# Kernel tuning notes

Measured on AMD Instinct MI355X. Metric: run time of the kernel, lower is better.

The kernel has to match this reference:

```python
import jax, jax.numpy as jnp
import numpy as np

B, S, D, V, T, NS, NG = 16, 512, 400, 32000, 8, 30, 3


def setup_inputs() -> dict:
    key = jax.random.key(0)
    ks = jax.random.split(key, 14)
    w = 1.0 / np.sqrt(D)
    return {
        "encoded_hidden": jax.random.normal(ks[0], (1, B, D), jnp.float32) * 0.1,
        "encoded_outputs": jax.random.normal(ks[1], (B, S, D), jnp.float32) * 0.1,
        "story": jax.random.randint(ks[2], (B, S), 0, V),
        "trg_batches": jax.random.randint(ks[3], (B, NS, T), 0, V),
        "shared_emb": jax.random.normal(ks[4], (V, D), jnp.float32) * 0.1,
        "slot_emb": jax.random.normal(ks[5], (1, D), jnp.float32) * 0.1,
        "w_ih": jax.random.normal(ks[6], (3 * D, D), jnp.float32) * w,
        "w_hh": jax.random.normal(ks[7], (3 * D, D), jnp.float32) * w,
        "b_ih": jax.random.normal(ks[8], (3 * D,), jnp.float32) * w,
        "b_hh": jax.random.normal(ks[9], (3 * D,), jnp.float32) * w,
        "w_ratio_w": jax.random.normal(ks[10], (1, 3 * D), jnp.float32) * w,
        "w_ratio_b": jax.random.normal(ks[11], (1,), jnp.float32) * w,
        "w_gate_w": jax.random.normal(ks[12], (NG, D), jnp.float32) * w,
        "w_gate_b": jax.random.normal(ks[13], (NG,), jnp.float32) * w,
        "batch_size": B,
        "max_resp_len": T,
    }


def reference(encoded_hidden, encoded_outputs, story, trg_batches, shared_emb,
              slot_emb, w_ih, w_hh, b_ih, b_hh, w_ratio_w, w_ratio_b,
              w_gate_w, w_gate_b, batch_size, max_resp_len):
    # Original torch code returns inside the slot loop -> only slot 0 is decoded.
    # h0 is re-used as GRU initial state at EVERY step (no carried hidden), and
    # teacher forcing makes each step's input known, so all T steps vectorize.
    h0 = encoded_hidden[0]                         # (B, D)
    Bq, Tq = batch_size, max_resp_len
    Vq = shared_emb.shape[0]

    # decoder inputs: step 0 = slot embedding, steps 1..T-1 = emb(trg[:,0,i-1])
    x0 = jnp.broadcast_to(slot_emb, h0.shape)      # (B, D)
    xt = shared_emb[trg_batches[:, 0, : Tq - 1]]   # (B, T-1, D)
    X = jnp.concatenate([x0[:, None, :], xt], axis=1)  # (B, T, D)

    # GRU cell (torch gate order r, z, n), h0 broadcast over steps
    gi = X @ w_ih.T + b_ih                         # (B, T, 3D)
    gh = h0 @ w_hh.T + b_hh                        # (B, 3D)
    i_r, i_z, i_n = jnp.split(gi, 3, axis=-1)
    h_r, h_z, h_n = jnp.split(gh, 3, axis=-1)
    r = jax.nn.sigmoid(i_r + h_r[:, None, :])
    z = jax.nn.sigmoid(i_z + h_z[:, None, :])
    n = jnp.tanh(i_n + r * h_n[:, None, :])
    h = (1.0 - z) * n + z * h0[:, None, :]         # (B, T, D) decoder_state == hidden

    # attention over history (no length masking: all lens == S)
    scores = jnp.einsum('btd,bsd->bts', h, encoded_outputs)   # (B, T, S)
    probs = jax.nn.softmax(scores, axis=-1)
    # FAITHFUL to original bug: context uses raw scores, not probs
    context = jnp.einsum('bts,bsd->btd', scores, encoded_outputs)

    gate0 = context[:, 0, :] @ w_gate_w.T + w_gate_b          # (B, NG), step i==0

    p_vocab = jax.nn.softmax(h @ shared_emb.T, axis=-1)       # (B, T, V)
    p_gen = jax.nn.sigmoid(
        jnp.concatenate([h, context, X], axis=-1) @ w_ratio_w.T + w_ratio_b
    )                                                         # (B, T, 1)

    # pointer distribution: scatter_add probs onto vocab ids of the story
    p_ctx = jnp.zeros((Bq, Tq, Vq), p_vocab.dtype).at[
        jnp.arange(Bq)[:, None, None],
        jnp.arange(Tq)[None, :, None],
        story[:, None, :],
    ].add(probs)

    p_final = p_gen * p_vocab + (1.0 - p_gen) * p_ctx         # (B, T, V)

    ptr_outputs = jnp.zeros((NS, Bq, Tq, Vq), p_final.dtype).at[0].set(p_final)
    gate_outputs = jnp.zeros((NS, Bq, NG), gate0.dtype).at[0].set(gate0)
    return ptr_outputs, gate_outputs
```

## Files before the change

### kernel.cpp

```cpp
#include <hip/hip_runtime.h>

#define Bq 16
#define Sq 512
#define Dq 400
#define Vq 32000
#define Tq 8
#define NSq 30
#define NGq 3
#define BTq (Bq*Tq)
#define SLICE 4096000
#define PTR_TOTAL (30ull*SLICE)
#define GATE_TOTAL (NSq*Bq*NGq)

#define ZTOT 29696000ull
#define ZPER 16384
#define AZB 640
#define LZB 1173

#define NCOMPUTE 250

#define FBLK 8
#define FCH (Vq/FBLK)

typedef float f4nt __attribute__((ext_vector_type(4)));

__device__ inline float sigmoidf_(float x) { return 1.0f / (1.0f + __expf(-x)); }

__device__ inline unsigned bf16rne(float x) {
    unsigned u = __float_as_uint(x);
    return (u + 0x7FFFu + ((u >> 16) & 1u)) >> 16;
}

__device__ inline float blockReduceSum(float v, float* red) {
    int tid = threadIdx.x;
    #pragma unroll
    for (int o = 32; o > 0; o >>= 1) v += __shfl_down(v, o, 64);
    if ((tid & 63) == 0) red[tid >> 6] = v;
    __syncthreads();
    if (tid == 0) {
        float s = red[0];
        int nw = blockDim.x >> 6;
        for (int i = 1; i < nw; i++) s += red[i];
        red[0] = s;
    }
    __syncthreads();
    float r = red[0];
    __syncthreads();
    return r;
}

__device__ inline float blockReduceMax(float v, float* red) {
    int tid = threadIdx.x;
    #pragma unroll
    for (int o = 32; o > 0; o >>= 1) v = fmaxf(v, __shfl_down(v, o, 64));
    if ((tid & 63) == 0) red[tid >> 6] = v;
    __syncthreads();
    if (tid == 0) {
        float s = red[0];
        int nw = blockDim.x >> 6;
        for (int i = 1; i < nw; i++) s = fmaxf(s, red[i]);
        red[0] = s;
    }
    __syncthreads();
    float r = red[0];
    __syncthreads();
    return r;
}

__global__ __launch_bounds__(512) void k_attn(const float* __restrict__ enc_hidden,
                                              const float* __restrict__ shared_emb,
                                              const float* __restrict__ slot_emb,
                                              const float* __restrict__ w_ih,
                                              const float* __restrict__ w_hh,
                                              const float* __restrict__ b_ih,
                                              const float* __restrict__ b_hh,
                                              const int* __restrict__ trg,
                                              const float* __restrict__ enc_out,
                                              const int* __restrict__ story,
                                              const float* __restrict__ w_ratio_w,
                                              const float* __restrict__ w_ratio_b,
                                              const float* __restrict__ w_gate_w,
                                              const float* __restrict__ w_gate_b,
                                              float* __restrict__ probs, float* __restrict__ pgen,
                                              float* __restrict__ hT, float* __restrict__ out_gate,
                                              float* __restrict__ out) {
    int tid = threadIdx.x;
    if (blockIdx.x >= BTq) {
        int zb = blockIdx.x - BTq;
        f4nt z = (f4nt)(0.0f);
        f4nt* dst = (f4nt*)(out + (size_t)SLICE);
        size_t base = (size_t)zb * ZPER + tid;
        #pragma unroll
        for (int r = 0; r < ZPER / 512; ++r) {
            size_t idx = base + (size_t)r * 512;
            if (idx < ZTOT) __builtin_nontemporal_store(z, &dst[idx]);
        }
        return;
    }
    __shared__ float x_l[Dq], h0_l[Dq], h_l[Dq], ctx_l[Dq], sc_l[Sq];
    __shared__ float gi_l[1200], gh_l[1200];
    __shared__ float red[8];
    int bt = blockIdx.x, b = bt >> 3, t = bt & 7;
    if (tid < 100) {
        const float4* src = (t == 0) ? (const float4*)slot_emb
            : (const float4*)(shared_emb + (size_t)trg[b * (NSq * Tq) + (t - 1)] * Dq);
        *(float4*)&x_l[4 * tid] = src[tid];
    } else if (tid >= 256 && tid < 356) {
        int q = tid - 256;
        *(float4*)&h0_l[4 * q] = ((const float4*)(enc_hidden + b * Dq))[q];
    }
    __syncthreads();
    for (int j = tid; j < 1200; j += 512) {
        const float4* wi4 = (const float4*)(w_ih + (size_t)j * Dq);
        const float4* wh4 = (const float4*)(w_hh + (size_t)j * Dq);
        const float4* x4  = (const float4*)x_l;
        const float4* h4  = (const float4*)h0_l;
        float ai = b_ih[j], ah = b_hh[j];
        #pragma unroll 4
        for (int q = 0; q < Dq / 4; ++q) {
            float4 wv = wi4[q], av = x4[q];
            ai += av.x * wv.x + av.y * wv.y + av.z * wv.z + av.w * wv.w;
            float4 wh = wh4[q], hv = h4[q];
            ah += hv.x * wh.x + hv.y * wh.y + hv.z * wh.z + hv.w * wh.w;
        }
        gi_l[j] = ai; gh_l[j] = ah;
    }
    __syncthreads();
    if (tid < Dq) {
        int d = tid;
        float r_ = sigmoidf_(gi_l[d] + gh_l[d]);
        float z  = sigmoidf_(gi_l[Dq + d] + gh_l[Dq + d]);
        float n  = tanhf(gi_l[2 * Dq + d] + r_ * gh_l[2 * Dq + d]);
        float h  = (1.0f - z) * n + z * h0_l[d];
        h_l[d] = h;
        hT[d * BTq + bt] = h;
    }
    __syncthreads();
    {
        const float4* e4 = (const float4*)(enc_out + ((size_t)(b * Sq + tid)) * Dq);
        float acc = 0.0f;
        for (int q = 0; q < Dq / 4; ++q) {
            float4 p = e4[q];
            int k = 4 * q;
            acc += h_l[k]*p.x + h_l[k+1]*p.y + h_l[k+2]*p.z + h_l[k+3]*p.w;
        }
        sc_l[tid] = acc;
    }
    __syncthreads();
    float myv = sc_l[tid];
    float m = blockReduceMax(myv, red);
    float e = __expf(myv - m);
    float ssum = blockReduceSum(e, red);
    probs[bt * Sq + tid] = e / ssum;
    for (int d = tid; d < Dq; d += 512) {
        float acc = 0.0f;
        #pragma unroll 8
        for (int s = 0; s < Sq; ++s)
            acc += sc_l[s] * enc_out[((size_t)(b * Sq + s)) * Dq + d];
        ctx_l[d] = acc;
    }
    __syncthreads();
    {
        float part = 0.0f;
        for (int i = tid; i < 1200; i += 512) {
            float v = (i < Dq) ? h_l[i] : (i < 2 * Dq ? ctx_l[i - Dq] : x_l[i - 2 * Dq]);
            part += v * w_ratio_w[i];
        }
        float tot = blockReduceSum(part, red);
        if (tid == 0) pgen[bt] = sigmoidf_(tot + w_ratio_b[0]);
    }
    if (t == 0) {
        for (int g = 0; g < NGq; ++g) {
            float part = 0.0f;
            for (int d = tid; d < Dq; d += 512) part += ctx_l[d] * w_gate_w[g * Dq + d];
            float tot = blockReduceSum(part, red);
            if (tid == 0) out_gate[b * NGq + g] = tot + w_gate_b[g];
        }
    }
}

#define TVL 128
#define CKL 40
__global__ __launch_bounds__(256) void k_logits(const float* __restrict__ hT,
                                                const float* __restrict__ emb,
                                                unsigned short* __restrict__ logits,
                                                float* __restrict__ pmax,
                                                float* __restrict__ psum,
                                                float* __restrict__ out) {
    __shared__ float eT[CKL][132];
    __shared__ float hL[CKL][132];
    int bid = blockIdx.x;
    int tid = threadIdx.x;
    if (bid >= NCOMPUTE) {
        int zl = bid - NCOMPUTE;
        if (zl < LZB) {
            int zb = AZB + zl;
            f4nt z = (f4nt)(0.0f);
            f4nt* dst = (f4nt*)(out + (size_t)SLICE);
            size_t base = (size_t)zb * ZPER + tid;
            #pragma unroll
            for (int r = 0; r < ZPER / 256; ++r) {
                size_t idx = base + (size_t)r * 256;
                if (idx < ZTOT) __builtin_nontemporal_store(z, &dst[idx]);
            }
        } else {
            float4 z4 = make_float4(0.0f, 0.0f, 0.0f, 0.0f);
            float4* g = (float4*)(out + PTR_TOTAL + Bq * NGq);
            for (int i = tid; i < (GATE_TOTAL - Bq * NGq) / 4; i += 256) g[i] = z4;
        }
        return;
    }
    int v0 = bid * TVL;
    int tx = tid & 15, ty = tid >> 4;
    float acc[8][8];
    #pragma unroll
    for (int j = 0; j < 8; ++j)
        #pragma unroll
        for (int i = 0; i < 8; ++i) acc[j][i] = 0.0f;

    for (int c = 0; c < Dq / CKL; ++c) {
        int k0 = c * CKL;
        const float4* hg = (const float4*)(hT + (size_t)k0 * BTq);
        #pragma unroll
        for (int r = 0; r < 5; ++r) {
            int idx = tid + 256 * r;
            int k = idx >> 5, c4 = idx & 31;
            float4 vd = hg[idx];
            *(float4*)&hL[k][4 * c4] = vd;
        }
        #pragma unroll
        for (int r = 0; r < 5; ++r) {
            int idx = tid + 256 * r;
            int v = idx / 10, q = idx - 10 * v;
            float4 vd = *(const float4*)(emb + (size_t)(v0 + v) * Dq + k0 + 4 * q);
            eT[4*q+0][v] = vd.x; eT[4*q+1][v] = vd.y; eT[4*q+2][v] = vd.z; eT[4*q+3][v] = vd.w;
        }
        __syncthreads();
        #pragma unroll 4
        for (int k = 0; k < CKL; ++k) {
            float4 h0 = *(const float4*)&hL[k][8 * ty];
            float4 h1 = *(const float4*)&hL[k][8 * ty + 4];
            float4 e0 = *(const float4*)&eT[k][8 * tx];
            float4 e1 = *(const float4*)&eT[k][8 * tx + 4];
            float hv[8] = {h0.x, h0.y, h0.z, h0.w, h1.x, h1.y, h1.z, h1.w};
            float ev[8] = {e0.x, e0.y, e0.z, e0.w, e1.x, e1.y, e1.z, e1.w};
            #pragma unroll
            for (int j = 0; j < 8; ++j)
                #pragma unroll
                for (int i = 0; i < 8; ++i)
                    acc[j][i] += hv[j] * ev[i];
        }
        __syncthreads();
    }
    #pragma unroll
    for (int j = 0; j < 8; ++j) {
        int bt = 8 * ty + j;
        unsigned bb[8];
        float r[8];
        float m = -1e30f;
        #pragma unroll
        for (int i = 0; i < 8; ++i) {
            bb[i] = bf16rne(acc[j][i]);
            r[i] = __uint_as_float(bb[i] << 16);
            m = fmaxf(m, r[i]);
        }
        #pragma unroll
        for (int o = 8; o >= 1; o >>= 1) m = fmaxf(m, __shfl_xor(m, o, 16));
        float es = 0.0f;
        #pragma unroll
        for (int i = 0; i < 8; ++i) es += __expf(r[i] - m);
        #pragma unroll
        for (int o = 8; o >= 1; o >>= 1) es += __shfl_xor(es, o, 16);
        if (tx == 0) {
            pmax[bid * BTq + bt] = m;
            psum[bid * BTq + bt] = es;
        }
        uint4 w = make_uint4(bb[0] | (bb[1] << 16), bb[2] | (bb[3] << 16),
                             bb[4] | (bb[5] << 16), bb[6] | (bb[7] << 16));
        *(uint4*)(logits + (size_t)bt * Vq + v0 + 8 * tx) = w;
    }
}

__global__ __launch_bounds__(256) void k_final(const unsigned short* __restrict__ logits,
                                               const float* __restrict__ probs,
                                               const int* __restrict__ story,
                                               const float* __restrict__ pgen,
                                               const float* __restrict__ pmax,
                                               const float* __restrict__ psum,
                                               float* __restrict__ out) {
    __shared__ float chunk[FCH];
    __shared__ float red[4];
    int bid = blockIdx.x, tid = threadIdx.x;
    int bt = bid >> 3, ch = bid & 7, b = bt >> 3;
    float pm = (tid < NCOMPUTE) ? pmax[tid * BTq + bt] : -1e30f;
    float m = blockReduceMax(pm, red);
    float part = (tid < NCOMPUTE) ? psum[tid * BTq + bt] * __expf(pm - m) : 0.0f;
    float s = blockReduceSum(part, red);
    float inv = 1.0f / s, pg = pgen[bt], cg = 1.0f - pg;
    int lo = ch * FCH;
    const uint4* l4 = (const uint4*)(logits + (size_t)bt * Vq + lo);
    for (int i = tid; i < FCH / 8; i += 256) {
        uint4 lv = l4[i];
        float f0 = __uint_as_float(lv.x << 16), f1 = __uint_as_float(lv.x & 0xFFFF0000u);
        float f2 = __uint_as_float(lv.y << 16), f3 = __uint_as_float(lv.y & 0xFFFF0000u);
        float f4 = __uint_as_float(lv.z << 16), f5 = __uint_as_float(lv.z & 0xFFFF0000u);
        float f6 = __uint_as_float(lv.w << 16), f7 = __uint_as_float(lv.w & 0xFFFF0000u);
        chunk[8 * i + 0] = pg * __expf(f0 - m) * inv;
        chunk[8 * i + 1] = pg * __expf(f1 - m) * inv;
        chunk[8 * i + 2] = pg * __expf(f2 - m) * inv;
        chunk[8 * i + 3] = pg * __expf(f3 - m) * inv;
        chunk[8 * i + 4] = pg * __expf(f4 - m) * inv;
        chunk[8 * i + 5] = pg * __expf(f5 - m) * inv;
        chunk[8 * i + 6] = pg * __expf(f6 - m) * inv;
        chunk[8 * i + 7] = pg * __expf(f7 - m) * inv;
    }
    __syncthreads();
    for (int ss = tid; ss < Sq; ss += 256) {
        int rel = story[b * Sq + ss] - lo;
        if (rel >= 0 && rel < FCH)
            atomicAdd(&chunk[rel], cg * probs[bt * Sq + ss]);
    }
    __syncthreads();
    f4nt* o4 = (f4nt*)(out + (size_t)bt * Vq + lo);
    const f4nt* c4 = (const f4nt*)chunk;
    for (int i = tid; i < FCH / 4; i += 256)
        __builtin_nontemporal_store(c4[i], &o4[i]);
}

extern "C" void kernel_launch(void* const* d_in, const int* in_sizes, int n_in,
                              void* d_out, int out_size, void* d_ws, size_t ws_size,
                              hipStream_t stream) {
    const float* enc_hidden = (const float*)d_in[0];
    const float* enc_out    = (const float*)d_in[1];
    const int*   story      = (const int*)d_in[2];
    const int*   trg        = (const int*)d_in[3];
    const float* shared_emb = (const float*)d_in[4];
    const float* slot_emb   = (const float*)d_in[5];
    const float* w_ih       = (const float*)d_in[6];
    const float* w_hh       = (const float*)d_in[7];
    const float* b_ih       = (const float*)d_in[8];
    const float* b_hh       = (const float*)d_in[9];
    const float* w_ratio_w  = (const float*)d_in[10];
    const float* w_ratio_b  = (const float*)d_in[11];
    const float* w_gate_w   = (const float*)d_in[12];
    const float* w_gate_b   = (const float*)d_in[13];

    float* out = (float*)d_out;

    float* ws = (float*)d_ws;
    unsigned short* logits_buf = (unsigned short*)ws;
    float* probs_buf  = ws + (size_t)SLICE;
    float* hT_buf     = ws + 2 * (size_t)SLICE;
    float* pgen_buf   = hT_buf + 51200;
    float* pmax_buf   = pgen_buf + 128;
    float* psum_buf   = pmax_buf + 32000;

    hipLaunchKernelGGL(k_attn, dim3(BTq + AZB), dim3(512), 0, stream,
                       enc_hidden, shared_emb, slot_emb, w_ih, w_hh, b_ih, b_hh, trg,
                       enc_out, story, w_ratio_w, w_ratio_b, w_gate_w, w_gate_b,
                       probs_buf, pgen_buf, hT_buf, out + PTR_TOTAL, out);
    hipLaunchKernelGGL(k_logits, dim3(NCOMPUTE + LZB + 1), dim3(256), 0, stream,
                       hT_buf, shared_emb, logits_buf, pmax_buf, psum_buf, out);
    hipLaunchKernelGGL(k_final, dim3(BTq * FBLK), dim3(256), 0, stream,
                       logits_buf, probs_buf, story, pgen_buf, pmax_buf, psum_buf, out);
}
```

Baseline: 735.7 us.

## Fuse logits and final softmax/scatter via cooperative grid sync, drop bf16 logits buffer

Merges the logits GEMM and the final softmax-plus-pointer-scatter kernel into one cooperative kernel. Logits stay in registers across a grid-wide sync, so the bf16 logits buffer no longer has to be written and re-read. Each block reduces the global max/sum, then applies the softmax, does the story scatter into its 128-wide vocab slice and writes the output. The zero-fill blocks become a fixed grid-stride set that also joins the grid sync. The costs are a cooperative launch with a limit on grid size, a grid barrier, and a per-block scatter loop over all 128 rows × 512 story tokens.

```diff
diff --git a/kernel.cpp b/kernel.cpp
--- a/kernel.cpp
+++ b/kernel.cpp
@@ -1,4 +1,5 @@
 #include <hip/hip_runtime.h>
+#include <hip/hip_cooperative_groups.h>
 
 #define Bq 16
 #define Sq 512
@@ -15,12 +16,11 @@
 #define ZTOT 29696000ull
 #define ZPER 16384
 #define AZB 640
-#define LZB 1173
+#define ZSTART (640ull*16384ull)
 
 #define NCOMPUTE 250
-
-#define FBLK 8
-#define FCH (Vq/FBLK)
+#define NZB 262
+#define ZSTRIDE (NZB*256)
 
 typedef float f4nt __attribute__((ext_vector_type(4)));
 
@@ -181,38 +181,39 @@
 
 #define TVL 128
 #define CKL 40
-__global__ __launch_bounds__(256) void k_logits(const float* __restrict__ hT,
-                                                const float* __restrict__ emb,
-                                                unsigned short* __restrict__ logits,
-                                                float* __restrict__ pmax,
-                                                float* __restrict__ psum,
-                                                float* __restrict__ out) {
-    __shared__ float eT[CKL][132];
-    __shared__ float hL[CKL][132];
+__global__ __launch_bounds__(256, 2) void k_logits(const float* __restrict__ hT,
+                                                   const float* __restrict__ emb,
+                                                   const float* __restrict__ probs,
+                                                   const int* __restrict__ story,
+                                                   const float* __restrict__ pgen,
+                                                   float* __restrict__ pmax,
+                                                   float* __restrict__ psum,
+                                                   float* __restrict__ out) {
+    namespace cg = cooperative_groups;
+    __shared__ __align__(16) float smem[16384];
     int bid = blockIdx.x;
     int tid = threadIdx.x;
+    int tx = tid & 15, ty = tid >> 4;
+    int v0 = bid * TVL;
+    float acc[8][8];
+
     if (bid >= NCOMPUTE) {
-        int zl = bid - NCOMPUTE;
-        if (zl < LZB) {
-            int zb = AZB + zl;
-            f4nt z = (f4nt)(0.0f);
-            f4nt* dst = (f4nt*)(out + (size_t)SLICE);
-            size_t base = (size_t)zb * ZPER + tid;
-            #pragma unroll
-            for (int r = 0; r < ZPER / 256; ++r) {
-                size_t idx = base + (size_t)r * 256;
-                if (idx < ZTOT) __builtin_nontemporal_store(z, &dst[idx]);
-            }
-        } else {
+        int zb = bid - NCOMPUTE;
+        f4nt z = (f4nt)(0.0f);
+        f4nt* dst = (f4nt*)(out + (size_t)SLICE);
+        for (size_t idx = ZSTART + (size_t)zb * 256 + tid; idx < ZTOT; idx += ZSTRIDE)
+            __builtin_nontemporal_store(z, &dst[idx]);
+        if (zb == 0) {
             float4 z4 = make_float4(0.0f, 0.0f, 0.0f, 0.0f);
             float4* g = (float4*)(out + PTR_TOTAL + Bq * NGq);
             for (int i = tid; i < (GATE_TOTAL - Bq * NGq) / 4; i += 256) g[i] = z4;
         }
+        cg::this_grid().sync();
         return;
     }
-    int v0 = bid * TVL;
-    int tx = tid & 15, ty = tid >> 4;
-    float acc[8][8];
+
+    float (*eT)[132] = (float(*)[132])smem;
+    float (*hL)[132] = (float(*)[132])(smem + 5280);
     #pragma unroll
     for (int j = 0; j < 8; ++j)
         #pragma unroll
@@ -255,76 +256,84 @@
     #pragma unroll
     for (int j = 0; j < 8; ++j) {
         int bt = 8 * ty + j;
-        unsigned bb[8];
-        float r[8];
         float m = -1e30f;
         #pragma unroll
         for (int i = 0; i < 8; ++i) {
-            bb[i] = bf16rne(acc[j][i]);
-            r[i] = __uint_as_float(bb[i] << 16);
-            m = fmaxf(m, r[i]);
+            unsigned bb = bf16rne(acc[j][i]);
+            acc[j][i] = __uint_as_float(bb << 16);
+            m = fmaxf(m, acc[j][i]);
         }
         #pragma unroll
         for (int o = 8; o >= 1; o >>= 1) m = fmaxf(m, __shfl_xor(m, o, 16));
         float es = 0.0f;
         #pragma unroll
-        for (int i = 0; i < 8; ++i) es += __expf(r[i] - m);
+        for (int i = 0; i < 8; ++i) es += __expf(acc[j][i] - m);
         #pragma unroll
         for (int o = 8; o >= 1; o >>= 1) es += __shfl_xor(es, o, 16);
         if (tx == 0) {
-            pmax[bid * BTq + bt] = m;
-            psum[bid * BTq + bt] = es;
-        }
-        uint4 w = make_uint4(bb[0] | (bb[1] << 16), bb[2] | (bb[3] << 16),
-                             bb[4] | (bb[5] << 16), bb[6] | (bb[7] << 16));
-        *(uint4*)(logits + (size_t)bt * Vq + v0 + 8 * tx) = w;
-    }
-}
-
-__global__ __launch_bounds__(256) void k_final(const unsigned short* __restrict__ logits,
-                                               const float* __restrict__ probs,
-                                               const int* __restrict__ story,
-                                               const float* __restrict__ pgen,
-                                               const float* __restrict__ pmax,
-                                               const float* __restrict__ psum,
-                                               float* __restrict__ out) {
-    __shared__ float chunk[FCH];
-    __shared__ float red[4];
-    int bid = blockIdx.x, tid = threadIdx.x;
-    int bt = bid >> 3, ch = bid & 7, b = bt >> 3;
-    float pm = (tid < NCOMPUTE) ? pmax[tid * BTq + bt] : -1e30f;
-    float m = blockReduceMax(pm, red);
-    float part = (tid < NCOMPUTE) ? psum[tid * BTq + bt] * __expf(pm - m) : 0.0f;
-    float s = blockReduceSum(part, red);
-    float inv = 1.0f / s, pg = pgen[bt], cg = 1.0f - pg;
-    int lo = ch * FCH;
-    const uint4* l4 = (const uint4*)(logits + (size_t)bt * Vq + lo);
-    for (int i = tid; i < FCH / 8; i += 256) {
-        uint4 lv = l4[i];
-        float f0 = __uint_as_float(lv.x << 16), f1 = __uint_as_float(lv.x & 0xFFFF0000u);
-        float f2 = __uint_as_float(lv.y << 16), f3 = __uint_as_float(lv.y & 0xFFFF0000u);
-        float f4 = __uint_as_float(lv.z << 16), f5 = __uint_as_float(lv.z & 0xFFFF0000u);
-        float f6 = __uint_as_float(lv.w << 16), f7 = __uint_as_float(lv.w & 0xFFFF0000u);
-        chunk[8 * i + 0] = pg * __expf(f0 - m) * inv;
-        chunk[8 * i + 1] = pg * __expf(f1 - m) * inv;
-        chunk[8 * i + 2] = pg * __expf(f2 - m) * inv;
-        chunk[8 * i + 3] = pg * __expf(f3 - m) * inv;
-        chunk[8 * i + 4] = pg * __expf(f4 - m) * inv;
-        chunk[8 * i + 5] = pg * __expf(f5 - m) * inv;
-        chunk[8 * i + 6] = pg * __expf(f6 - m) * inv;
-        chunk[8 * i + 7] = pg * __expf(f7 - m) * inv;
-    }
-    __syncthreads();
-    for (int ss = tid; ss < Sq; ss += 256) {
-        int rel = story[b * Sq + ss] - lo;
-        if (rel >= 0 && rel < FCH)
-            atomicAdd(&chunk[rel], cg * probs[bt * Sq + ss]);
-    }
-    __syncthreads();
-    f4nt* o4 = (f4nt*)(out + (size_t)bt * Vq + lo);
-    const f4nt* c4 = (const f4nt*)chunk;
-    for (int i = tid; i < FCH / 4; i += 256)
-        __builtin_nontemporal_store(c4[i], &o4[i]);
+            pmax[bt * 256 + bid] = m;
+            psum[bt * 256 + bid] = es;
+        }
+    }
+
+    cg::this_grid().sync();
+
+    {
+        int wave = tid >> 6, lane = tid & 63;
+        for (int r = wave; r < BTq; r += 4) {
+            float pmv[4]; float m = -1e30f;
+            #pragma unroll
+            for (int k = 0; k < 4; ++k) {
+                int idx = lane + 64 * k;
+                pmv[k] = (idx < NCOMPUTE) ? pmax[r * 256 + idx] : -1e30f;
+                m = fmaxf(m, pmv[k]);
+            }
+            #pragma unroll
+            for (int o = 32; o > 0; o >>= 1) m = fmaxf(m, __shfl_xor(m, o, 64));
+            float s = 0.0f;
+            #pragma unroll
+            for (int k = 0; k < 4; ++k) {
+                int idx = lane + 64 * k;
+                if (idx < NCOMPUTE) s += psum[r * 256 + idx] * __expf(pmv[k] - m);
+            }
+            #pragma unroll
+            for (int o = 32; o > 0; o >>= 1) s += __shfl_xor(s, o, 64);
+            if (lane == 0) { smem[r] = m; smem[128 + r] = s; }
+        }
+    }
+    __syncthreads();
+    float rm[8], ri[8], rpg[8];
+    #pragma unroll
+    for (int j = 0; j < 8; ++j) {
+        int bt = 8 * ty + j;
+        rm[j] = smem[bt];
+        ri[j] = 1.0f / smem[128 + bt];
+        rpg[j] = pgen[bt];
+    }
+    __syncthreads();
+    #pragma unroll
+    for (int j = 0; j < 8; ++j) {
+        int bt = 8 * ty + j;
+        #pragma unroll
+        for (int i = 0; i < 8; ++i)
+            smem[bt * 128 + 8 * tx + i] = rpg[j] * __expf(acc[j][i] - rm[j]) * ri[j];
+    }
+    __syncthreads();
+    for (int r = 0; r < BTq; ++r) {
+        int b = r >> 3;
+        float cg = 1.0f - pgen[r];
+        for (int s = tid; s < Sq; s += 256) {
+            int rel = story[b * Sq + s] - v0;
+            if ((unsigned)rel < 128u)
+                atomicAdd(&smem[r * 128 + rel], cg * probs[r * Sq + s]);
+        }
+    }
+    __syncthreads();
+    for (int i = tid; i < BTq * 32; i += 256) {
+        int r = i >> 5, q = i & 31;
+        f4nt v = *(f4nt*)&smem[r * 128 + 4 * q];
+        __builtin_nontemporal_store(v, (f4nt*)(out + (size_t)r * Vq + v0 + 4 * q));
+    }
 }
 
 extern "C" void kernel_launch(void* const* d_in, const int* in_sizes, int n_in,
@@ -348,19 +357,20 @@
     float* out = (float*)d_out;
 
     float* ws = (float*)d_ws;
-    unsigned short* logits_buf = (unsigned short*)ws;
-    float* probs_buf  = ws + (size_t)SLICE;
-    float* hT_buf     = ws + 2 * (size_t)SLICE;
-    float* pgen_buf   = hT_buf + 51200;
-    float* pmax_buf   = pgen_buf + 128;
-    float* psum_buf   = pmax_buf + 32000;
+    float* probs_buf = ws;
+    float* hT_buf    = probs_buf + 65536;
+    float* pgen_buf  = hT_buf + 51200;
+    float* pmax_buf  = pgen_buf + 128;
+    float* psum_buf  = pmax_buf + 32768;
 
     hipLaunchKernelGGL(k_attn, dim3(BTq + AZB), dim3(512), 0, stream,
                        enc_hidden, shared_emb, slot_emb, w_ih, w_hh, b_ih, b_hh, trg,
                        enc_out, story, w_ratio_w, w_ratio_b, w_gate_w, w_gate_b,
                        probs_buf, pgen_buf, hT_buf, out + PTR_TOTAL, out);
-    hipLaunchKernelGGL(k_logits, dim3(NCOMPUTE + LZB + 1), dim3(256), 0, stream,
-                       hT_buf, shared_emb, logits_buf, pmax_buf, psum_buf, out);
-    hipLaunchKernelGGL(k_final, dim3(BTq * FBLK), dim3(256), 0, stream,
-                       logits_buf, probs_buf, story, pgen_buf, pmax_buf, psum_buf, out);
-}
+
+    void* args[] = {(void*)&hT_buf, (void*)&shared_emb, (void*)&probs_buf,
+                    (void*)&story, (void*)&pgen_buf, (void*)&pmax_buf,
+                    (void*)&psum_buf, (void*)&out};
+    hipLaunchCooperativeKernel((const void*)k_logits, dim3(NCOMPUTE + NZB), dim3(256),
+                               args, 0, stream);
+}
```

New measurement: 883.0 us. 1.2x slower.

## Move attention stage into logits kernel to overlap with vocab GEMM

Applied to the files above, without the earlier changes.

Splits the first kernel so it only computes the GRU hidden state, writing both a transposed and a row-major copy. The attention scores, softmax, context, p_gen and gate computations move into extra blocks of the logits kernel, so they run alongside the vocabulary GEMM instead of sitting on the critical path before it. The zero-fill split between the two kernels is rebalanced to match. This costs an extra hidden-state buffer, and the attention now runs with 256-thread blocks that share dynamic shared memory with the GEMM tiles.

```diff
diff --git a/kernel.cpp b/kernel.cpp
--- a/kernel.cpp
+++ b/kernel.cpp
@@ -14,10 +14,11 @@
 
 #define ZTOT 29696000ull
 #define ZPER 16384
-#define AZB 640
-#define LZB 1173
+#define AZB1 400
+#define LZB2 1413
 
 #define NCOMPUTE 250
+#define NATTN 128
 
 #define FBLK 8
 #define FCH (Vq/FBLK)
@@ -67,23 +68,16 @@
     return r;
 }
 
-__global__ __launch_bounds__(512) void k_attn(const float* __restrict__ enc_hidden,
-                                              const float* __restrict__ shared_emb,
-                                              const float* __restrict__ slot_emb,
-                                              const float* __restrict__ w_ih,
-                                              const float* __restrict__ w_hh,
-                                              const float* __restrict__ b_ih,
-                                              const float* __restrict__ b_hh,
-                                              const int* __restrict__ trg,
-                                              const float* __restrict__ enc_out,
-                                              const int* __restrict__ story,
-                                              const float* __restrict__ w_ratio_w,
-                                              const float* __restrict__ w_ratio_b,
-                                              const float* __restrict__ w_gate_w,
-                                              const float* __restrict__ w_gate_b,
-                                              float* __restrict__ probs, float* __restrict__ pgen,
-                                              float* __restrict__ hT, float* __restrict__ out_gate,
-                                              float* __restrict__ out) {
+__global__ __launch_bounds__(512) void k_gru(const float* __restrict__ enc_hidden,
+                                             const float* __restrict__ shared_emb,
+                                             const float* __restrict__ slot_emb,
+                                             const float* __restrict__ w_ih,
+                                             const float* __restrict__ w_hh,
+                                             const float* __restrict__ b_ih,
+                                             const float* __restrict__ b_hh,
+                                             const int* __restrict__ trg,
+                                             float* __restrict__ hT, float* __restrict__ hB,
+                                             float* __restrict__ out) {
     int tid = threadIdx.x;
     if (blockIdx.x >= BTq) {
         int zb = blockIdx.x - BTq;
@@ -97,9 +91,8 @@
         }
         return;
     }
-    __shared__ float x_l[Dq], h0_l[Dq], h_l[Dq], ctx_l[Dq], sc_l[Sq];
+    __shared__ float x_l[Dq], h0_l[Dq];
     __shared__ float gi_l[1200], gh_l[1200];
-    __shared__ float red[8];
     int bt = blockIdx.x, b = bt >> 3, t = bt & 7;
     if (tid < 100) {
         const float4* src = (t == 0) ? (const float4*)slot_emb
@@ -132,50 +125,8 @@
         float z  = sigmoidf_(gi_l[Dq + d] + gh_l[Dq + d]);
         float n  = tanhf(gi_l[2 * Dq + d] + r_ * gh_l[2 * Dq + d]);
         float h  = (1.0f - z) * n + z * h0_l[d];
-        h_l[d] = h;
         hT[d * BTq + bt] = h;
-    }
-    __syncthreads();
-    {
-        const float4* e4 = (const float4*)(enc_out + ((size_t)(b * Sq + tid)) * Dq);
-        float acc = 0.0f;
-        for (int q = 0; q < Dq / 4; ++q) {
-            float4 p = e4[q];
-            int k = 4 * q;
-            acc += h_l[k]*p.x + h_l[k+1]*p.y + h_l[k+2]*p.z + h_l[k+3]*p.w;
-        }
-        sc_l[tid] = acc;
-    }
-    __syncthreads();
-    float myv = sc_l[tid];
-    float m = blockReduceMax(myv, red);
-    float e = __expf(myv - m);
-    float ssum = blockReduceSum(e, red);
-    probs[bt * Sq + tid] = e / ssum;
-    for (int d = tid; d < Dq; d += 512) {
-        float acc = 0.0f;
-        #pragma unroll 8
-        for (int s = 0; s < Sq; ++s)
-            acc += sc_l[s] * enc_out[((size_t)(b * Sq + s)) * Dq + d];
-        ctx_l[d] = acc;
-    }
-    __syncthreads();
-    {
-        float part = 0.0f;
-        for (int i = tid; i < 1200; i += 512) {
-            float v = (i < Dq) ? h_l[i] : (i < 2 * Dq ? ctx_l[i - Dq] : x_l[i - 2 * Dq]);
-            part += v * w_ratio_w[i];
-        }
-        float tot = blockReduceSum(part, red);
-        if (tid == 0) pgen[bt] = sigmoidf_(tot + w_ratio_b[0]);
-    }
-    if (t == 0) {
-        for (int g = 0; g < NGq; ++g) {
-            float part = 0.0f;
-            for (int d = tid; d < Dq; d += 512) part += ctx_l[d] * w_gate_w[g * Dq + d];
-            float tot = blockReduceSum(part, red);
-            if (tid == 0) out_gate[b * NGq + g] = tot + w_gate_b[g];
-        }
+        hB[bt * Dq + d]  = h;
     }
 }
 
@@ -183,18 +134,90 @@
 #define CKL 40
 __global__ __launch_bounds__(256) void k_logits(const float* __restrict__ hT,
                                                 const float* __restrict__ emb,
+                                                const float* __restrict__ hB,
+                                                const float* __restrict__ slot_emb,
+                                                const int* __restrict__ trg,
+                                                const float* __restrict__ enc_out,
+                                                const float* __restrict__ w_ratio_w,
+                                                const float* __restrict__ w_ratio_b,
+                                                const float* __restrict__ w_gate_w,
+                                                const float* __restrict__ w_gate_b,
+                                                float* __restrict__ probs,
+                                                float* __restrict__ pgen,
+                                                float* __restrict__ out_gate,
                                                 unsigned short* __restrict__ logits,
                                                 float* __restrict__ pmax,
                                                 float* __restrict__ psum,
                                                 float* __restrict__ out) {
-    __shared__ float eT[CKL][132];
-    __shared__ float hL[CKL][132];
+    __shared__ __align__(16) float smem[10560];
     int bid = blockIdx.x;
     int tid = threadIdx.x;
+
     if (bid >= NCOMPUTE) {
-        int zl = bid - NCOMPUTE;
-        if (zl < LZB) {
-            int zb = AZB + zl;
+        int r0 = bid - NCOMPUTE;
+        if (r0 < NATTN) {
+            float* h_l  = smem;
+            float* ctx_l= smem + 400;
+            float* x_l  = smem + 800;
+            float* sc_l = smem + 1200;
+            float* red  = smem + 1712;
+            int bt = r0, b = bt >> 3, t = bt & 7;
+            if (tid < 100) {
+                *(float4*)&h_l[4 * tid] = ((const float4*)(hB + (size_t)bt * Dq))[tid];
+            } else if (tid < 200) {
+                int q = tid - 100;
+                const float4* src = (t == 0) ? (const float4*)slot_emb
+                    : (const float4*)(emb + (size_t)trg[b * (NSq * Tq) + (t - 1)] * Dq);
+                *(float4*)&x_l[4 * q] = src[q];
+            }
+            __syncthreads();
+            for (int s = tid; s < Sq; s += 256) {
+                const float4* e4 = (const float4*)(enc_out + ((size_t)(b * Sq + s)) * Dq);
+                float acc = 0.0f;
+                for (int q = 0; q < Dq / 4; ++q) {
+                    float4 p = e4[q];
+                    int k = 4 * q;
+                    acc += h_l[k]*p.x + h_l[k+1]*p.y + h_l[k+2]*p.z + h_l[k+3]*p.w;
+                }
+                sc_l[s] = acc;
+            }
+            __syncthreads();
+            float v0 = sc_l[tid], v1 = sc_l[tid + 256];
+            float m = blockReduceMax(fmaxf(v0, v1), red);
+            float e0 = __expf(v0 - m), e1 = __expf(v1 - m);
+            float ssum = blockReduceSum(e0 + e1, red);
+            probs[bt * Sq + tid]       = e0 / ssum;
+            probs[bt * Sq + tid + 256] = e1 / ssum;
+            for (int d = tid; d < Dq; d += 256) {
+                float acc = 0.0f;
+                #pragma unroll 8
+                for (int s = 0; s < Sq; ++s)
+                    acc += sc_l[s] * enc_out[((size_t)(b * Sq + s)) * Dq + d];
+                ctx_l[d] = acc;
+            }
+            __syncthreads();
+            {
+                float part = 0.0f;
+                for (int i = tid; i < 1200; i += 256) {
+                    float v = (i < Dq) ? h_l[i] : (i < 2 * Dq ? ctx_l[i - Dq] : x_l[i - 2 * Dq]);
+                    part += v * w_ratio_w[i];
+                }
+                float tot = blockReduceSum(part, red);
+                if (tid == 0) pgen[bt] = sigmoidf_(tot + w_ratio_b[0]);
+            }
+            if (t == 0) {
+                for (int g = 0; g < NGq; ++g) {
+                    float part = 0.0f;
+                    for (int d = tid; d < Dq; d += 256) part += ctx_l[d] * w_gate_w[g * Dq + d];
+                    float tot = blockReduceSum(part, red);
+                    if (tid == 0) out_gate[b * NGq + g] = tot + w_gate_b[g];
+                }
+            }
+            return;
+        }
+        int zl = r0 - NATTN;
+        if (zl < LZB2) {
+            int zb = AZB1 + zl;
             f4nt z = (f4nt)(0.0f);
             f4nt* dst = (f4nt*)(out + (size_t)SLICE);
             size_t base = (size_t)zb * ZPER + tid;
@@ -210,6 +233,9 @@
         }
         return;
     }
+
+    float (*eT)[132] = (float(*)[132])smem;
+    float (*hL)[132] = (float(*)[132])(smem + 5280);
     int v0 = bid * TVL;
     int tx = tid & 15, ty = tid >> 4;
     float acc[8][8];
@@ -349,18 +375,21 @@
 
     float* ws = (float*)d_ws;
     unsigned short* logits_buf = (unsigned short*)ws;
-    float* probs_buf  = ws + (size_t)SLICE;
-    float* hT_buf     = ws + 2 * (size_t)SLICE;
-    float* pgen_buf   = hT_buf + 51200;
-    float* pmax_buf   = pgen_buf + 128;
-    float* psum_buf   = pmax_buf + 32000;
-
-    hipLaunchKernelGGL(k_attn, dim3(BTq + AZB), dim3(512), 0, stream,
+    float* probs_buf = ws + (size_t)SLICE;
+    float* hT_buf    = probs_buf + 65536;
+    float* hB_buf    = hT_buf + 51200;
+    float* pgen_buf  = hB_buf + 51200;
+    float* pmax_buf  = pgen_buf + 128;
+    float* psum_buf  = pmax_buf + 32000;
+
+    hipLaunchKernelGGL(k_gru, dim3(BTq + AZB1), dim3(512), 0, stream,
                        enc_hidden, shared_emb, slot_emb, w_ih, w_hh, b_ih, b_hh, trg,
-                       enc_out, story, w_ratio_w, w_ratio_b, w_gate_w, w_gate_b,
-                       probs_buf, pgen_buf, hT_buf, out + PTR_TOTAL, out);
-    hipLaunchKernelGGL(k_logits, dim3(NCOMPUTE + LZB + 1), dim3(256), 0, stream,
-                       hT_buf, shared_emb, logits_buf, pmax_buf, psum_buf, out);
+                       hT_buf, hB_buf, out);
+    hipLaunchKernelGGL(k_logits, dim3(NCOMPUTE + NATTN + LZB2 + 1), dim3(256), 0, stream,
+                       hT_buf, shared_emb, hB_buf, slot_emb, trg, enc_out,
+                       w_ratio_w, w_ratio_b, w_gate_w, w_gate_b,
+                       probs_buf, pgen_buf, out + PTR_TOTAL,
+                       logits_buf, pmax_buf, psum_buf, out);
     hipLaunchKernelGGL(k_final, dim3(BTq * FBLK), dim3(256), 0, stream,
                        logits_buf, probs_buf, story, pgen_buf, pmax_buf, psum_buf, out);
 }
```

Result: no change. 722.7 us (-1.8%).
